# Kernel optimization log

Measured on AMD Instinct MI355X. Metric: run time of the kernel, lower is better.

Reference implementation:

```python
import jax, jax.numpy as jnp
import numpy as np

B, S, D, UNITS = 4, 512, 256, 128
NEG = -1e9


def setup_inputs() -> dict:
    key = jax.random.key(0)
    k1, k2, k3, k4 = jax.random.split(key, 4)
    values = jax.random.normal(k1, (B, S, D), dtype=jnp.float32)
    Wq = jax.random.normal(k2, (D, UNITS), dtype=jnp.float32) * (1.0 / np.sqrt(D))
    Wv = jax.random.normal(k3, (D, UNITS), dtype=jnp.float32) * (1.0 / np.sqrt(D))
    Vw = jax.random.normal(k4, (UNITS,), dtype=jnp.float32) * (1.0 / np.sqrt(UNITS))
    return {"values": values, "Wq": Wq, "Wv": Wv, "Vw": Vw}


def reference(values, Wq, Wv, Vw):
    # values: [B, S, D]
    query = values @ Wq            # [B, S, U]
    value = values @ Wv            # [B, S, U]
    # additive (Bahdanau) score: V . tanh(q_i + v_j) -> [B, S, S]
    feat = jnp.tanh(query[:, :, None, :] + value[:, None, :, :])  # [B,S,S,U]
    score = jnp.einsum('biju,u->bij', feat, Vw)
    seq_len = values.shape[1]
    causal = jnp.tril(jnp.ones((seq_len, seq_len), dtype=jnp.float32))  # lower-tri = visible
    score = score + (1.0 - causal)[None, :, :] * jnp.asarray(NEG, score.dtype)
    attn = jax.nn.softmax(score, axis=-1)          # [B, S, S]
    context = jnp.matmul(attn, values)             # [B, S, D]
    return context
```

## Files before the change

### kernel.cpp

```cpp
#include <hip/hip_runtime.h>
#include <hip/hip_fp16.h>

#define SEQ 512
#define DIM 256
#define UN  128
#define BSZ 2048
#define CSC 2.8853900817779268f

struct h4v { __half2 a, b; };

static __device__ __forceinline__ unsigned short f2bf(float x) {
  unsigned u = __float_as_uint(x);
  u += 0x7FFF + ((u >> 16) & 1);
  return (unsigned short)(u >> 16);
}
static __device__ __forceinline__ float bf2f(unsigned short s) {
  return __uint_as_float((unsigned)s << 16);
}
static __device__ __forceinline__ float rdlane(float v, int k) {
  return __int_as_float(__builtin_amdgcn_readlane(__float_as_int(v), k));
}

__global__ __launch_bounds__(256) void proj_kernel(
    const float* __restrict__ values, const float* __restrict__ Wq,
    const float* __restrict__ Wv, float* __restrict__ Eq,
    unsigned short* __restrict__ Ev, __half* __restrict__ Vf16) {
  __shared__ float vsm[4 * DIM];
  const int t = threadIdx.x;
  const int r0 = blockIdx.x * 4;
  {
    const int row = t >> 6, c4 = (t & 63) * 4;
    const float4 v = *(const float4*)(values + (r0 + row) * DIM + c4);
    *(float4*)&vsm[row * DIM + c4] = v;
    __half2* vf = (__half2*)(Vf16 + (r0 + row) * DIM + c4);
    vf[0] = __floats2half2_rn(v.x, v.y);
    vf[1] = __floats2half2_rn(v.z, v.w);
  }
  __syncthreads();
  const int half = t >> 7, u = t & 127;
  const float* __restrict__ W = half ? Wv : Wq;
  float acc[4] = {0.f, 0.f, 0.f, 0.f};
  for (int d = 0; d < DIM; d += 4) {
    const float w0 = W[(d + 0) * UN + u], w1 = W[(d + 1) * UN + u];
    const float w2 = W[(d + 2) * UN + u], w3 = W[(d + 3) * UN + u];
#pragma unroll
    for (int k = 0; k < 4; ++k) {
      const float4 v = *(const float4*)&vsm[k * DIM + d];
      acc[k] = fmaf(v.x, w0, acc[k]);
      acc[k] = fmaf(v.y, w1, acc[k]);
      acc[k] = fmaf(v.z, w2, acc[k]);
      acc[k] = fmaf(v.w, w3, acc[k]);
    }
  }
  if (!half) {
#pragma unroll
    for (int k = 0; k < 4; ++k)
      Eq[(r0 + k) * UN + u] = __builtin_amdgcn_exp2f(acc[k] * CSC);
  } else {
    ushort4 o;
    o.x = f2bf(__builtin_amdgcn_exp2f(acc[0] * CSC));
    o.y = f2bf(__builtin_amdgcn_exp2f(acc[1] * CSC));
    o.z = f2bf(__builtin_amdgcn_exp2f(acc[2] * CSC));
    o.w = f2bf(__builtin_amdgcn_exp2f(acc[3] * CSC));
    *(ushort4*)(Ev + (size_t)u * BSZ + r0) = o;
  }
}

__global__ __launch_bounds__(256, 4) void attn_kernel(
    const __half* __restrict__ Vf16, const float* __restrict__ Eq,
    const unsigned short* __restrict__ Ev, const float* __restrict__ Vw,
    float* __restrict__ out) {
  __shared__ float sc[2 * SEQ];
  __shared__ float scp[2 * SEQ];
  __shared__ float part[8 * DIM];
  __shared__ float invs[2];

  const int t = threadIdx.x;
  const int lane = t & 63;
  const int b = blockIdx.x >> 8, p = blockIdx.x & 255;
  const int bS = b * SEQ;
  const int i = p;
  const int ihi = SEQ - 1 - p;
  const int jhi = ihi;

  const float* __restrict__ eql = Eq + (size_t)(bS + i) * UN;
  const float* __restrict__ eqh = Eq + (size_t)(bS + ihi) * UN;
  const int u0 = (t >> 7) << 6;

  const float qhv = eqh[u0 + lane];
  const float qlv = eql[u0 + lane];
  const float wv  = Vw[u0 + lane];

  {
    const int qd = t & 127, jb = qd << 2;
    float* __restrict__ so = (t >> 7) ? scp : sc;
    const unsigned short* __restrict__ evp = Ev + (size_t)u0 * BSZ + bS + jb;
#define LDE(K) (*(const ushort4*)(evp + (size_t)(K) * BSZ))
    if ((t & 64) == 0) {
      float h0=0.f,h1=0.f,h2=0.f,h3=0.f,l0=0.f,l1=0.f,l2=0.f,l3=0.f;
      ushort4 e0 = LDE(0), e1 = LDE(1), e2 = LDE(2), e3 = LDE(3);
#define PRD(EC, KK) { \
      const float qh = rdlane(qhv, (KK)); \
      const float ql = rdlane(qlv, (KK)); \
      const float w  = rdlane(wv,  (KK)); \
      const float f0 = bf2f(EC.x), f1 = bf2f(EC.y), f2 = bf2f(EC.z), f3 = bf2f(EC.w); \
      h0 = fmaf(w, __builtin_amdgcn_rcpf(fmaf(qh, f0, 1.f)), h0); \
      h1 = fmaf(w, __builtin_amdgcn_rcpf(fmaf(qh, f1, 1.f)), h1); \
      h2 = fmaf(w, __builtin_amdgcn_rcpf(fmaf(qh, f2, 1.f)), h2); \
      h3 = fmaf(w, __builtin_amdgcn_rcpf(fmaf(qh, f3, 1.f)), h3); \
      l0 = fmaf(w, __builtin_amdgcn_rcpf(fmaf(ql, f0, 1.f)), l0); \
      l1 = fmaf(w, __builtin_amdgcn_rcpf(fmaf(ql, f1, 1.f)), l1); \
      l2 = fmaf(w, __builtin_amdgcn_rcpf(fmaf(ql, f2, 1.f)), l2); \
      l3 = fmaf(w, __builtin_amdgcn_rcpf(fmaf(ql, f3, 1.f)), l3); }
      for (int k = 0; k < 64; k += 4) {
        ushort4 n;
        n = LDE(k + 4); PRD(e0, k + 0); e0 = n;
        n = LDE(k + 5); PRD(e1, k + 1); e1 = n;
        n = LDE(k + 6); PRD(e2, k + 2); e2 = n;
        n = LDE(k + 7); PRD(e3, k + 3); e3 = n;
      }
#undef PRD
      *(float4*)&so[SEQ + jb] = make_float4(h0, h1, h2, h3);
      *(float4*)&so[jb]       = make_float4(l0, l1, l2, l3);
    } else if (jb <= jhi) {
      float h0=0.f,h1=0.f,h2=0.f,h3=0.f;
      ushort4 e0 = LDE(0), e1 = LDE(1), e2 = LDE(2), e3 = LDE(3);
#define PRS(EC, KK) { \
      const float qh = rdlane(qhv, (KK)); \
      const float w  = rdlane(wv,  (KK)); \
      h0 = fmaf(w, __builtin_amdgcn_rcpf(fmaf(qh, bf2f(EC.x), 1.f)), h0); \
      h1 = fmaf(w, __builtin_amdgcn_rcpf(fmaf(qh, bf2f(EC.y), 1.f)), h1); \
      h2 = fmaf(w, __builtin_amdgcn_rcpf(fmaf(qh, bf2f(EC.z), 1.f)), h2); \
      h3 = fmaf(w, __builtin_amdgcn_rcpf(fmaf(qh, bf2f(EC.w), 1.f)), h3); }
      for (int k = 0; k < 64; k += 4) {
        ushort4 n;
        n = LDE(k + 4); PRS(e0, k + 0); e0 = n;
        n = LDE(k + 5); PRS(e1, k + 1); e1 = n;
        n = LDE(k + 6); PRS(e2, k + 2); e2 = n;
        n = LDE(k + 7); PRS(e3, k + 3); e3 = n;
      }
#undef PRS
      *(float4*)&so[SEQ + jb] = make_float4(h0, h1, h2, h3);
    }
#undef LDE
  }
  __syncthreads();

  {
    const int w = t >> 6, l = lane;
    if (w == 0) {
      float m = 1e30f;
      for (int j = l; j <= i; j += 64) m = fminf(m, sc[j] + scp[j]);
#pragma unroll
      for (int o = 32; o; o >>= 1) m = fminf(m, __shfl_xor(m, o));
      float sum = 0.f;
      for (int j = l; j < 256; j += 64) {
        if (j <= i) {
          const float pr = __builtin_amdgcn_exp2f((m - (sc[j] + scp[j])) * CSC);
          sc[j] = pr; sum += pr;
        } else {
          sc[j] = 0.f;
        }
      }
#pragma unroll
      for (int o = 32; o; o >>= 1) sum += __shfl_xor(sum, o);
      if (l == 0) invs[0] = __builtin_amdgcn_rcpf(sum);
    } else if (w == 1) {
      float m = 1e30f;
      for (int j = l; j <= jhi; j += 64) m = fminf(m, sc[SEQ + j] + scp[SEQ + j]);
#pragma unroll
      for (int o = 32; o; o >>= 1) m = fminf(m, __shfl_xor(m, o));
      float sum = 0.f;
      for (int j = l; j <= jhi; j += 64) {
        const float pr = __builtin_amdgcn_exp2f((m - (sc[SEQ + j] + scp[SEQ + j])) * CSC);
        sc[SEQ + j] = pr; sum += pr;
      }
#pragma unroll
      for (int o = 32; o; o >>= 1) sum += __shfl_xor(sum, o);
      if (l == 0) invs[1] = __builtin_amdgcn_rcpf(sum);
    }
  }
  __syncthreads();

  {
    const int g = t >> 6;
    const int d4 = lane << 2;
    const float plo0 = sc[g + (lane << 2)];
    const float phi0 = sc[SEQ + g + (lane << 2)];
    const float phi1 = sc[SEQ + 256 + g + (lane << 2)];
    float a0=0.f,a1=0.f,a2=0.f,a3=0.f, c0=0.f,c1=0.f,c2=0.f,c3=0.f;
    const __half* __restrict__ vb = Vf16 + (size_t)bS * DIM + d4;
    h4v vc = *(const h4v*)(vb + g * DIM);
#pragma unroll 8
    for (int k = 0; k < 64; ++k) {
      const h4v vn = *(const h4v*)(vb + (size_t)(g + 4 * k + 4) * DIM);
      const float pl = rdlane(plo0, k), ph = rdlane(phi0, k);
      const float2 f01 = __half22float2(vc.a), f23 = __half22float2(vc.b);
      a0 = fmaf(pl, f01.x, a0); a1 = fmaf(pl, f01.y, a1);
      a2 = fmaf(pl, f23.x, a2); a3 = fmaf(pl, f23.y, a3);
      c0 = fmaf(ph, f01.x, c0); c1 = fmaf(ph, f01.y, c1);
      c2 = fmaf(ph, f23.x, c2); c3 = fmaf(ph, f23.y, c3);
      vc = vn;
    }
    int k2 = 0;
#pragma unroll 4
    for (int j = g + 256; j <= jhi; j += 4, ++k2) {
      const int jn = (j + 4 <= jhi) ? j + 4 : jhi;
      const h4v vn = *(const h4v*)(vb + (size_t)jn * DIM);
      const float ph = rdlane(phi1, k2);
      const float2 f01 = __half22float2(vc.a), f23 = __half22float2(vc.b);
      c0 = fmaf(ph, f01.x, c0); c1 = fmaf(ph, f01.y, c1);
      c2 = fmaf(ph, f23.x, c2); c3 = fmaf(ph, f23.y, c3);
      vc = vn;
    }
    *(float4*)&part[(g * 2 + 0) * DIM + d4] = make_float4(a0, a1, a2, a3);
    *(float4*)&part[(g * 2 + 1) * DIM + d4] = make_float4(c0, c1, c2, c3);
  }
  __syncthreads();

  {
    const float olo = (part[0 * DIM + t] + part[2 * DIM + t] +
                       part[4 * DIM + t] + part[6 * DIM + t]) * invs[0];
    const float ohi = (part[1 * DIM + t] + part[3 * DIM + t] +
                       part[5 * DIM + t] + part[7 * DIM + t]) * invs[1];
    out[(size_t)(bS + i) * DIM + t] = olo;
    out[(size_t)(bS + ihi) * DIM + t] = ohi;
  }
}

extern "C" void kernel_launch(void* const* d_in, const int* in_sizes, int n_in,
                              void* d_out, int out_size, void* d_ws, size_t ws_size,
                              hipStream_t stream) {
  const float* values = (const float*)d_in[0];
  const float* Wq     = (const float*)d_in[1];
  const float* Wv     = (const float*)d_in[2];
  const float* Vw     = (const float*)d_in[3];
  float* out = (float*)d_out;
  float* Eq = (float*)d_ws;
  unsigned short* Ev = (unsigned short*)(Eq + (size_t)BSZ * UN);
  __half* Vf16 = (__half*)(Ev + (size_t)UN * BSZ);
  proj_kernel<<<dim3(BSZ / 4), 256, 0, stream>>>(values, Wq, Wv, Eq, Ev, Vf16);
  attn_kernel<<<dim3(4 * 256), 256, 0, stream>>>(Vf16, Eq, Ev, Vw, out);
}
```

Baseline: 111.6 us.

## Split attention into score and context kernels with balanced unit split

Splits the fused attention kernel into a score kernel and a context kernel, with normalized probabilities passed through a new fp16 P buffer in workspace. In the score kernel each of the four waves now owns 32 hidden units for all key positions, instead of two warps split by row half. This replaces the old imbalance where the low-row wave did twice the work of the others. Softmax now runs across all 256 threads with cross-wave reductions. The cost is an extra launch, a global write and read of P, and fp16 rounding of the probabilities.

```diff
diff --git a/kernel.cpp b/kernel.cpp
--- a/kernel.cpp
+++ b/kernel.cpp
@@ -66,17 +66,15 @@
   }
 }
 
-__global__ __launch_bounds__(256, 4) void attn_kernel(
-    const __half* __restrict__ Vf16, const float* __restrict__ Eq,
-    const unsigned short* __restrict__ Ev, const float* __restrict__ Vw,
-    float* __restrict__ out) {
-  __shared__ float sc[2 * SEQ];
-  __shared__ float scp[2 * SEQ];
-  __shared__ float part[8 * DIM];
-  __shared__ float invs[2];
+__global__ __launch_bounds__(256, 4) void score_kernel(
+    const float* __restrict__ Eq, const unsigned short* __restrict__ Ev,
+    const float* __restrict__ Vw, __half* __restrict__ P) {
+  __shared__ float slo[4 * 256];
+  __shared__ float shi[4 * SEQ];
+  __shared__ float red[16];
 
   const int t = threadIdx.x;
-  const int lane = t & 63;
+  const int l = t & 63, w = t >> 6;
   const int b = blockIdx.x >> 8, p = blockIdx.x & 255;
   const int bS = b * SEQ;
   const int i = p;
@@ -85,147 +83,155 @@
 
   const float* __restrict__ eql = Eq + (size_t)(bS + i) * UN;
   const float* __restrict__ eqh = Eq + (size_t)(bS + ihi) * UN;
-  const int u0 = (t >> 7) << 6;
-
-  const float qhv = eqh[u0 + lane];
-  const float qlv = eql[u0 + lane];
-  const float wv  = Vw[u0 + lane];
-
+  const int uq = w << 5;
+
+  const int lk = l & 31;
+  const float qlv = eql[uq + lk];
+  const float qhv = eqh[uq + lk];
+  const float wv  = Vw[uq + lk];
+
+#define LDE(PTR, K) (*(const ushort4*)((PTR) + (size_t)(K) * BSZ))
   {
-    const int qd = t & 127, jb = qd << 2;
-    float* __restrict__ so = (t >> 7) ? scp : sc;
-    const unsigned short* __restrict__ evp = Ev + (size_t)u0 * BSZ + bS + jb;
-#define LDE(K) (*(const ushort4*)(evp + (size_t)(K) * BSZ))
-    if ((t & 64) == 0) {
-      float h0=0.f,h1=0.f,h2=0.f,h3=0.f,l0=0.f,l1=0.f,l2=0.f,l3=0.f;
-      ushort4 e0 = LDE(0), e1 = LDE(1), e2 = LDE(2), e3 = LDE(3);
+    const unsigned short* __restrict__ evp = Ev + (size_t)uq * BSZ + bS + (l << 2);
+    float h0=0.f,h1=0.f,h2=0.f,h3=0.f,l0=0.f,l1=0.f,l2=0.f,l3=0.f;
+    ushort4 e0 = LDE(evp,0), e1 = LDE(evp,1), e2 = LDE(evp,2), e3 = LDE(evp,3);
 #define PRD(EC, KK) { \
-      const float qh = rdlane(qhv, (KK)); \
-      const float ql = rdlane(qlv, (KK)); \
-      const float w  = rdlane(wv,  (KK)); \
-      const float f0 = bf2f(EC.x), f1 = bf2f(EC.y), f2 = bf2f(EC.z), f3 = bf2f(EC.w); \
-      h0 = fmaf(w, __builtin_amdgcn_rcpf(fmaf(qh, f0, 1.f)), h0); \
-      h1 = fmaf(w, __builtin_amdgcn_rcpf(fmaf(qh, f1, 1.f)), h1); \
-      h2 = fmaf(w, __builtin_amdgcn_rcpf(fmaf(qh, f2, 1.f)), h2); \
-      h3 = fmaf(w, __builtin_amdgcn_rcpf(fmaf(qh, f3, 1.f)), h3); \
-      l0 = fmaf(w, __builtin_amdgcn_rcpf(fmaf(ql, f0, 1.f)), l0); \
-      l1 = fmaf(w, __builtin_amdgcn_rcpf(fmaf(ql, f1, 1.f)), l1); \
-      l2 = fmaf(w, __builtin_amdgcn_rcpf(fmaf(ql, f2, 1.f)), l2); \
-      l3 = fmaf(w, __builtin_amdgcn_rcpf(fmaf(ql, f3, 1.f)), l3); }
-      for (int k = 0; k < 64; k += 4) {
-        ushort4 n;
-        n = LDE(k + 4); PRD(e0, k + 0); e0 = n;
-        n = LDE(k + 5); PRD(e1, k + 1); e1 = n;
-        n = LDE(k + 6); PRD(e2, k + 2); e2 = n;
-        n = LDE(k + 7); PRD(e3, k + 3); e3 = n;
-      }
+    const float qh = rdlane(qhv, (KK)); \
+    const float ql = rdlane(qlv, (KK)); \
+    const float ww = rdlane(wv,  (KK)); \
+    const float f0 = bf2f(EC.x), f1 = bf2f(EC.y), f2 = bf2f(EC.z), f3 = bf2f(EC.w); \
+    h0 = fmaf(ww, __builtin_amdgcn_rcpf(fmaf(qh, f0, 1.f)), h0); \
+    h1 = fmaf(ww, __builtin_amdgcn_rcpf(fmaf(qh, f1, 1.f)), h1); \
+    h2 = fmaf(ww, __builtin_amdgcn_rcpf(fmaf(qh, f2, 1.f)), h2); \
+    h3 = fmaf(ww, __builtin_amdgcn_rcpf(fmaf(qh, f3, 1.f)), h3); \
+    l0 = fmaf(ww, __builtin_amdgcn_rcpf(fmaf(ql, f0, 1.f)), l0); \
+    l1 = fmaf(ww, __builtin_amdgcn_rcpf(fmaf(ql, f1, 1.f)), l1); \
+    l2 = fmaf(ww, __builtin_amdgcn_rcpf(fmaf(ql, f2, 1.f)), l2); \
+    l3 = fmaf(ww, __builtin_amdgcn_rcpf(fmaf(ql, f3, 1.f)), l3); }
+    for (int k = 0; k < 32; k += 4) {
+      ushort4 n;
+      n = LDE(evp, k + 4); PRD(e0, k + 0); e0 = n;
+      n = LDE(evp, k + 5); PRD(e1, k + 1); e1 = n;
+      n = LDE(evp, k + 6); PRD(e2, k + 2); e2 = n;
+      n = LDE(evp, k + 7); PRD(e3, k + 3); e3 = n;
+    }
 #undef PRD
-      *(float4*)&so[SEQ + jb] = make_float4(h0, h1, h2, h3);
-      *(float4*)&so[jb]       = make_float4(l0, l1, l2, l3);
-    } else if (jb <= jhi) {
-      float h0=0.f,h1=0.f,h2=0.f,h3=0.f;
-      ushort4 e0 = LDE(0), e1 = LDE(1), e2 = LDE(2), e3 = LDE(3);
+    *(float4*)&slo[(w << 8) + (l << 2)] = make_float4(l0, l1, l2, l3);
+    *(float4*)&shi[(w << 9) + (l << 2)] = make_float4(h0, h1, h2, h3);
+  }
+  if (256 + (l << 2) <= jhi) {
+    const unsigned short* __restrict__ evp = Ev + (size_t)uq * BSZ + bS + 256 + (l << 2);
+    float h0=0.f,h1=0.f,h2=0.f,h3=0.f;
+    ushort4 e0 = LDE(evp,0), e1 = LDE(evp,1), e2 = LDE(evp,2), e3 = LDE(evp,3);
 #define PRS(EC, KK) { \
-      const float qh = rdlane(qhv, (KK)); \
-      const float w  = rdlane(wv,  (KK)); \
-      h0 = fmaf(w, __builtin_amdgcn_rcpf(fmaf(qh, bf2f(EC.x), 1.f)), h0); \
-      h1 = fmaf(w, __builtin_amdgcn_rcpf(fmaf(qh, bf2f(EC.y), 1.f)), h1); \
-      h2 = fmaf(w, __builtin_amdgcn_rcpf(fmaf(qh, bf2f(EC.z), 1.f)), h2); \
-      h3 = fmaf(w, __builtin_amdgcn_rcpf(fmaf(qh, bf2f(EC.w), 1.f)), h3); }
-      for (int k = 0; k < 64; k += 4) {
-        ushort4 n;
-        n = LDE(k + 4); PRS(e0, k + 0); e0 = n;
-        n = LDE(k + 5); PRS(e1, k + 1); e1 = n;
-        n = LDE(k + 6); PRS(e2, k + 2); e2 = n;
-        n = LDE(k + 7); PRS(e3, k + 3); e3 = n;
-      }
+    const float qh = rdlane(qhv, (KK)); \
+    const float ww = rdlane(wv,  (KK)); \
+    h0 = fmaf(ww, __builtin_amdgcn_rcpf(fmaf(qh, bf2f(EC.x), 1.f)), h0); \
+    h1 = fmaf(ww, __builtin_amdgcn_rcpf(fmaf(qh, bf2f(EC.y), 1.f)), h1); \
+    h2 = fmaf(ww, __builtin_amdgcn_rcpf(fmaf(qh, bf2f(EC.z), 1.f)), h2); \
+    h3 = fmaf(ww, __builtin_amdgcn_rcpf(fmaf(qh, bf2f(EC.w), 1.f)), h3); }
+    for (int k = 0; k < 32; k += 4) {
+      ushort4 n;
+      n = LDE(evp, k + 4); PRS(e0, k + 0); e0 = n;
+      n = LDE(evp, k + 5); PRS(e1, k + 1); e1 = n;
+      n = LDE(evp, k + 6); PRS(e2, k + 2); e2 = n;
+      n = LDE(evp, k + 7); PRS(e3, k + 3); e3 = n;
+    }
 #undef PRS
-      *(float4*)&so[SEQ + jb] = make_float4(h0, h1, h2, h3);
-    }
+    *(float4*)&shi[(w << 9) + 256 + (l << 2)] = make_float4(h0, h1, h2, h3);
+  }
 #undef LDE
-  }
-  __syncthreads();
-
-  {
-    const int w = t >> 6, l = lane;
-    if (w == 0) {
-      float m = 1e30f;
-      for (int j = l; j <= i; j += 64) m = fminf(m, sc[j] + scp[j]);
-#pragma unroll
-      for (int o = 32; o; o >>= 1) m = fminf(m, __shfl_xor(m, o));
-      float sum = 0.f;
-      for (int j = l; j < 256; j += 64) {
-        if (j <= i) {
-          const float pr = __builtin_amdgcn_exp2f((m - (sc[j] + scp[j])) * CSC);
-          sc[j] = pr; sum += pr;
-        } else {
-          sc[j] = 0.f;
-        }
-      }
-#pragma unroll
-      for (int o = 32; o; o >>= 1) sum += __shfl_xor(sum, o);
-      if (l == 0) invs[0] = __builtin_amdgcn_rcpf(sum);
-    } else if (w == 1) {
-      float m = 1e30f;
-      for (int j = l; j <= jhi; j += 64) m = fminf(m, sc[SEQ + j] + scp[SEQ + j]);
-#pragma unroll
-      for (int o = 32; o; o >>= 1) m = fminf(m, __shfl_xor(m, o));
-      float sum = 0.f;
-      for (int j = l; j <= jhi; j += 64) {
-        const float pr = __builtin_amdgcn_exp2f((m - (sc[SEQ + j] + scp[SEQ + j])) * CSC);
-        sc[SEQ + j] = pr; sum += pr;
-      }
-#pragma unroll
-      for (int o = 32; o; o >>= 1) sum += __shfl_xor(sum, o);
-      if (l == 0) invs[1] = __builtin_amdgcn_rcpf(sum);
-    }
-  }
-  __syncthreads();
-
-  {
-    const int g = t >> 6;
-    const int d4 = lane << 2;
-    const float plo0 = sc[g + (lane << 2)];
-    const float phi0 = sc[SEQ + g + (lane << 2)];
-    const float phi1 = sc[SEQ + 256 + g + (lane << 2)];
-    float a0=0.f,a1=0.f,a2=0.f,a3=0.f, c0=0.f,c1=0.f,c2=0.f,c3=0.f;
-    const __half* __restrict__ vb = Vf16 + (size_t)bS * DIM + d4;
-    h4v vc = *(const h4v*)(vb + g * DIM);
+  __syncthreads();
+
+  const float sLo = slo[t] + slo[256 + t] + slo[512 + t] + slo[768 + t];
+  const float sHa = shi[t] + shi[512 + t] + shi[1024 + t] + shi[1536 + t];
+  const int t2 = 256 + t;
+  const float sHb = shi[t2] + shi[512 + t2] + shi[1024 + t2] + shi[1536 + t2];
+  const bool vLo = (t <= i);
+  const bool vHb = (t2 <= jhi);
+
+  float mLo = vLo ? sLo : 1e30f;
+  float mHi = fminf(sHa, vHb ? sHb : 1e30f);
+#pragma unroll
+  for (int o = 32; o; o >>= 1) {
+    mLo = fminf(mLo, __shfl_xor(mLo, o));
+    mHi = fminf(mHi, __shfl_xor(mHi, o));
+  }
+  if (l == 0) { red[w] = mLo; red[4 + w] = mHi; }
+  __syncthreads();
+  mLo = fminf(fminf(red[0], red[1]), fminf(red[2], red[3]));
+  mHi = fminf(fminf(red[4], red[5]), fminf(red[6], red[7]));
+
+  const float pLo = vLo ? __builtin_amdgcn_exp2f((mLo - sLo) * CSC) : 0.f;
+  const float pHa = __builtin_amdgcn_exp2f((mHi - sHa) * CSC);
+  const float pHb = vHb ? __builtin_amdgcn_exp2f((mHi - sHb) * CSC) : 0.f;
+  float suLo = pLo, suHi = pHa + pHb;
+#pragma unroll
+  for (int o = 32; o; o >>= 1) {
+    suLo += __shfl_xor(suLo, o);
+    suHi += __shfl_xor(suHi, o);
+  }
+  if (l == 0) { red[8 + w] = suLo; red[12 + w] = suHi; }
+  __syncthreads();
+  const float invLo = __builtin_amdgcn_rcpf(red[8] + red[9] + red[10] + red[11]);
+  const float invHi = __builtin_amdgcn_rcpf(red[12] + red[13] + red[14] + red[15]);
+
+  P[(size_t)(bS + i) * SEQ + t]   = __float2half(pLo * invLo);
+  P[(size_t)(bS + ihi) * SEQ + t] = __float2half(pHa * invHi);
+  if (vHb) P[(size_t)(bS + ihi) * SEQ + t2] = __float2half(pHb * invHi);
+}
+
+__global__ __launch_bounds__(256, 4) void ctx_kernel(
+    const __half* __restrict__ Vf16, const __half* __restrict__ P,
+    float* __restrict__ out) {
+  __shared__ float part[8 * DIM];
+  const int t = threadIdx.x, lane = t & 63, g = t >> 6;
+  const int b = blockIdx.x >> 8, p = blockIdx.x & 255;
+  const int bS = b * SEQ;
+  const int i = p, ihi = SEQ - 1 - p, jhi = ihi;
+
+  const __half* __restrict__ Plo = P + (size_t)(bS + i) * SEQ;
+  const __half* __restrict__ Phi = P + (size_t)(bS + ihi) * SEQ;
+  const int d4 = lane << 2;
+
+  const float plo0 = __half2float(Plo[g + (lane << 2)]);
+  const float phi0 = __half2float(Phi[g + (lane << 2)]);
+  const int j1 = 256 + g + (lane << 2);
+  const float phi1 = (j1 <= jhi) ? __half2float(Phi[j1]) : 0.f;
+
+  float a0=0.f,a1=0.f,a2=0.f,a3=0.f, c0=0.f,c1=0.f,c2=0.f,c3=0.f;
+  const __half* __restrict__ vb = Vf16 + (size_t)bS * DIM + d4;
+  h4v vc = *(const h4v*)(vb + g * DIM);
 #pragma unroll 8
-    for (int k = 0; k < 64; ++k) {
-      const h4v vn = *(const h4v*)(vb + (size_t)(g + 4 * k + 4) * DIM);
-      const float pl = rdlane(plo0, k), ph = rdlane(phi0, k);
-      const float2 f01 = __half22float2(vc.a), f23 = __half22float2(vc.b);
-      a0 = fmaf(pl, f01.x, a0); a1 = fmaf(pl, f01.y, a1);
-      a2 = fmaf(pl, f23.x, a2); a3 = fmaf(pl, f23.y, a3);
-      c0 = fmaf(ph, f01.x, c0); c1 = fmaf(ph, f01.y, c1);
-      c2 = fmaf(ph, f23.x, c2); c3 = fmaf(ph, f23.y, c3);
-      vc = vn;
-    }
-    int k2 = 0;
+  for (int k = 0; k < 64; ++k) {
+    const h4v vn = *(const h4v*)(vb + (size_t)(g + 4 * k + 4) * DIM);
+    const float pl = rdlane(plo0, k), ph = rdlane(phi0, k);
+    const float2 f01 = __half22float2(vc.a), f23 = __half22float2(vc.b);
+    a0 = fmaf(pl, f01.x, a0); a1 = fmaf(pl, f01.y, a1);
+    a2 = fmaf(pl, f23.x, a2); a3 = fmaf(pl, f23.y, a3);
+    c0 = fmaf(ph, f01.x, c0); c1 = fmaf(ph, f01.y, c1);
+    c2 = fmaf(ph, f23.x, c2); c3 = fmaf(ph, f23.y, c3);
+    vc = vn;
+  }
+  int k2 = 0;
 #pragma unroll 4
-    for (int j = g + 256; j <= jhi; j += 4, ++k2) {
-      const int jn = (j + 4 <= jhi) ? j + 4 : jhi;
-      const h4v vn = *(const h4v*)(vb + (size_t)jn * DIM);
-      const float ph = rdlane(phi1, k2);
-      const float2 f01 = __half22float2(vc.a), f23 = __half22float2(vc.b);
-      c0 = fmaf(ph, f01.x, c0); c1 = fmaf(ph, f01.y, c1);
-      c2 = fmaf(ph, f23.x, c2); c3 = fmaf(ph, f23.y, c3);
-      vc = vn;
-    }
-    *(float4*)&part[(g * 2 + 0) * DIM + d4] = make_float4(a0, a1, a2, a3);
-    *(float4*)&part[(g * 2 + 1) * DIM + d4] = make_float4(c0, c1, c2, c3);
-  }
-  __syncthreads();
-
-  {
-    const float olo = (part[0 * DIM + t] + part[2 * DIM + t] +
-                       part[4 * DIM + t] + part[6 * DIM + t]) * invs[0];
-    const float ohi = (part[1 * DIM + t] + part[3 * DIM + t] +
-                       part[5 * DIM + t] + part[7 * DIM + t]) * invs[1];
-    out[(size_t)(bS + i) * DIM + t] = olo;
-    out[(size_t)(bS + ihi) * DIM + t] = ohi;
-  }
+  for (int j = g + 256; j <= jhi; j += 4, ++k2) {
+    const int jn = (j + 4 <= jhi) ? j + 4 : jhi;
+    const h4v vn = *(const h4v*)(vb + (size_t)jn * DIM);
+    const float ph = rdlane(phi1, k2);
+    const float2 f01 = __half22float2(vc.a), f23 = __half22float2(vc.b);
+    c0 = fmaf(ph, f01.x, c0); c1 = fmaf(ph, f01.y, c1);
+    c2 = fmaf(ph, f23.x, c2); c3 = fmaf(ph, f23.y, c3);
+    vc = vn;
+  }
+  *(float4*)&part[(g * 2 + 0) * DIM + d4] = make_float4(a0, a1, a2, a3);
+  *(float4*)&part[(g * 2 + 1) * DIM + d4] = make_float4(c0, c1, c2, c3);
+  __syncthreads();
+
+  const float olo = part[t] + part[2 * DIM + t] + part[4 * DIM + t] + part[6 * DIM + t];
+  const float ohi = part[DIM + t] + part[3 * DIM + t] + part[5 * DIM + t] + part[7 * DIM + t];
+  out[(size_t)(bS + i) * DIM + t] = olo;
+  out[(size_t)(bS + ihi) * DIM + t] = ohi;
 }
 
 extern "C" void kernel_launch(void* const* d_in, const int* in_sizes, int n_in,
@@ -239,6 +245,8 @@
   float* Eq = (float*)d_ws;
   unsigned short* Ev = (unsigned short*)(Eq + (size_t)BSZ * UN);
   __half* Vf16 = (__half*)(Ev + (size_t)UN * BSZ);
+  __half* P = Vf16 + (size_t)BSZ * DIM;
   proj_kernel<<<dim3(BSZ / 4), 256, 0, stream>>>(values, Wq, Wv, Eq, Ev, Vf16);
-  attn_kernel<<<dim3(4 * 256), 256, 0, stream>>>(Vf16, Eq, Ev, Vw, out);
-}
+  score_kernel<<<dim3(4 * 256), 256, 0, stream>>>(Eq, Ev, Vw, P);
+  ctx_kernel<<<dim3(4 * 256), 256, 0, stream>>>(Vf16, P, out);
+}
```

After: 118.3 us. 1.06x slower.
